# Optimization experiments

Measured on AMD Instinct MI355X. Metric: run time of the kernel, lower is better.

The kernel has to match this reference:

```python
import jax, jax.numpy as jnp
import numpy as np

B, T, C = 8, 1024, 2048  # batch, seq_len (<= T_MAX=1024), n_embd == dim_att


def setup_inputs() -> dict:
    key = jax.random.key(0)
    ks = jax.random.split(key, 10)
    inp = {
        "x": jax.random.normal(ks[0], (B, T, C), dtype=jnp.float32),
        "time_decay": jax.random.normal(ks[1], (C,), dtype=jnp.float32),
        "time_first": jax.random.normal(ks[2], (C,), dtype=jnp.float32),
        "time_mix_k": jax.random.uniform(ks[3], (C,), dtype=jnp.float32),
        "time_mix_v": jax.random.uniform(ks[4], (C,), dtype=jnp.float32),
        "time_mix_r": jax.random.uniform(ks[5], (C,), dtype=jnp.float32),
        "Wk": jax.random.normal(ks[6], (C, C), dtype=jnp.float32) / np.sqrt(C),
        "Wv": jax.random.normal(ks[7], (C, C), dtype=jnp.float32) / np.sqrt(C),
        "Wr": jax.random.normal(ks[8], (C, C), dtype=jnp.float32) / np.sqrt(C),
        "Wo": jax.random.normal(ks[9], (C, C), dtype=jnp.float32) / np.sqrt(C),
    }
    return inp


def _wkv(time_decay, time_first, k, v):
    # Numerically-stabilized RWKV linear-attention recurrence (rwkv_linear_attention_cpu).
    # k, v: [B, T, C]; state tracked in float32.
    w = -jnp.exp(time_decay.astype(jnp.float32))  # [C]
    u = time_first.astype(jnp.float32)            # [C]
    kf = k.astype(jnp.float32)
    vf = v.astype(jnp.float32)

    def step(carry, kv):
        num, den, mx = carry           # each [B, C]
        kt, vt = kv                    # each [B, C]
        max_out = jnp.maximum(mx, kt + u)
        e1 = jnp.exp(mx - max_out)
        e2 = jnp.exp(kt + u - max_out)
        out = (e1 * num + e2 * vt) / (e1 * den + e2)
        max_st = jnp.maximum(mx + w, kt)
        e1s = jnp.exp(mx + w - max_st)
        e2s = jnp.exp(kt - max_st)
        return (e1s * num + e2s * vt, e1s * den + e2s, max_st), out

    Bn, Tn, Cn = k.shape
    init = (jnp.zeros((Bn, Cn), jnp.float32),
            jnp.zeros((Bn, Cn), jnp.float32),
            jnp.full((Bn, Cn), -1e38, jnp.float32))
    kT = jnp.swapaxes(kf, 0, 1)  # [T, B, C]
    vT = jnp.swapaxes(vf, 0, 1)
    _, outs = jax.lax.scan(step, init, (kT, vT))
    return jnp.swapaxes(outs, 0, 1).astype(k.dtype)  # [B, T, C]


def reference(x, time_decay, time_first, time_mix_k, time_mix_v, time_mix_r, Wk, Wv, Wr, Wo):
    # time_shift: shift sequence right by one, zero at t=0
    shifted = jnp.pad(x, ((0, 0), (1, 0), (0, 0)))[:, :-1]
    xk = x * time_mix_k + shifted * (1.0 - time_mix_k)
    xv = x * time_mix_v + shifted * (1.0 - time_mix_v)
    xr = x * time_mix_r + shifted * (1.0 - time_mix_r)
    k = jnp.einsum('btc,dc->btd', xk, Wk)
    v = jnp.einsum('btc,dc->btd', xv, Wv)
    r = jnp.einsum('btc,dc->btd', xr, Wr)
    sr = jax.nn.sigmoid(r)
    rwkv = _wkv(time_decay, time_first, k, v)
    return jnp.einsum('btd,cd->btc', sr * rwkv, Wo)
```

## Files before the change

### kernel.cpp

```cpp
#include <hip/hip_runtime.h>
#include <stdint.h>

#define B_DIM 8
#define T_DIM 1024
#define C_DIM 2048
#define M_DIM (B_DIM * T_DIM)
#define SEG   32
#define SEGL  (T_DIM / SEG)

typedef __bf16 bf16x8 __attribute__((ext_vector_type(8)));
typedef __bf16 bf16x4 __attribute__((ext_vector_type(4)));
typedef float  f32x4  __attribute__((ext_vector_type(4)));

__device__ __forceinline__ void gld_lds16(const void* g, void* l) {
    __builtin_amdgcn_global_load_lds((__attribute__((address_space(1))) void*)g,
                                     (__attribute__((address_space(3))) void*)l,
                                     16, 0, 0);
}

__global__ __launch_bounds__(256) void cast_w_kernel(
    const float* __restrict__ w0, const float* __restrict__ w1,
    const float* __restrict__ w2, const float* __restrict__ w3,
    __bf16* __restrict__ dst) {
    const float* srcs[4] = {w0, w1, w2, w3};
    const float* s = srcs[blockIdx.y];
    __bf16* d = dst + (size_t)blockIdx.y * (size_t)C_DIM * C_DIM;
    const size_t i = ((size_t)blockIdx.x * 256 + threadIdx.x) * 4;
    f32x4 v = *(const f32x4*)(s + i);
    bf16x4 o;
#pragma unroll
    for (int j = 0; j < 4; ++j) o[j] = (__bf16)v[j];
    *(bf16x4*)(d + i) = o;
}

__global__ __launch_bounds__(256) void mix4_kernel(
    const float* __restrict__ x,
    const float* __restrict__ mk, const float* __restrict__ mv,
    const float* __restrict__ mr,
    __bf16* __restrict__ xk, __bf16* __restrict__ xv, __bf16* __restrict__ xr) {
    const size_t idx = ((size_t)blockIdx.x * 256 + threadIdx.x) * 4;
    const int c = (int)(idx & (C_DIM - 1));
    const int t = (int)((idx >> 11) & (T_DIM - 1));

    f32x4 xc = *(const f32x4*)(x + idx);
    f32x4 sh = {0.f, 0.f, 0.f, 0.f};
    if (t != 0) sh = *(const f32x4*)(x + idx - C_DIM);
    f32x4 k4 = *(const f32x4*)(mk + c);
    f32x4 v4 = *(const f32x4*)(mv + c);
    f32x4 r4 = *(const f32x4*)(mr + c);

    bf16x4 ok, ov, orr;
#pragma unroll
    for (int j = 0; j < 4; ++j) {
        float xx = xc[j], ss = sh[j];
        ok[j]  = (__bf16)(xx * k4[j] + ss * (1.f - k4[j]));
        ov[j]  = (__bf16)(xx * v4[j] + ss * (1.f - v4[j]));
        orr[j] = (__bf16)(xx * r4[j] + ss * (1.f - r4[j]));
    }
    *(bf16x4*)(xk + idx) = ok;
    *(bf16x4*)(xv + idx) = ov;
    *(bf16x4*)(xr + idx) = orr;
}

#define LGKM(N)  do { asm volatile("s_waitcnt lgkmcnt(" #N ")" ::: "memory"); \
                      __builtin_amdgcn_sched_barrier(0); } while (0)
#define VM0()    asm volatile("s_waitcnt vmcnt(0)" ::: "memory")

#define MF1(mi, jj, AV, BV) \
    acc[mi][jj] = __builtin_amdgcn_mfma_f32_16x16x32_bf16(AV, BV, acc[mi][jj], 0, 0, 0)

#define MFMA16(MB, AA, BB)                                                        \
    __builtin_amdgcn_s_setprio(1);                                                \
    MF1(MB+0,0,AA[0],BB[0]); MF1(MB+0,1,AA[0],BB[1]);                             \
    MF1(MB+0,2,AA[0],BB[2]); MF1(MB+0,3,AA[0],BB[3]);                             \
    MF1(MB+1,0,AA[1],BB[0]); MF1(MB+1,1,AA[1],BB[1]);                             \
    MF1(MB+1,2,AA[1],BB[2]); MF1(MB+1,3,AA[1],BB[3]);                             \
    MF1(MB+2,0,AA[2],BB[0]); MF1(MB+2,1,AA[2],BB[1]);                             \
    MF1(MB+2,2,AA[2],BB[2]); MF1(MB+2,3,AA[2],BB[3]);                             \
    MF1(MB+3,0,AA[3],BB[0]); MF1(MB+3,1,AA[3],BB[1]);                             \
    MF1(MB+3,2,AA[3],BB[2]); MF1(MB+3,3,AA[3],BB[3]);                             \
    __builtin_amdgcn_s_setprio(0)

#define STAGE8(KOF, BOE)                                                          \
    do {                                                                          \
        gld_lds16(Ag + (KOF),                       lA + (BOE));                  \
        gld_lds16(Bg + (KOF),                       lB + (BOE));                  \
        gld_lds16(Ag + (KOF) + (size_t)64*C_DIM,    lA + (BOE) + 4096);           \
        gld_lds16(Bg + (KOF) + (size_t)64*C_DIM,    lB + (BOE) + 4096);           \
        gld_lds16(Ag + (KOF) + (size_t)128*C_DIM,   lA + (BOE) + 8192);           \
        gld_lds16(Bg + (KOF) + (size_t)128*C_DIM,   lB + (BOE) + 8192);           \
        gld_lds16(Ag + (KOF) + (size_t)192*C_DIM,   lA + (BOE) + 12288);          \
        gld_lds16(Bg + (KOF) + (size_t)192*C_DIM,   lB + (BOE) + 12288);          \
    } while (0)

template <bool OUTF32>
__global__ __launch_bounds__(512, 2) void gemm256_bt(
    const __bf16* __restrict__ A, const __bf16* __restrict__ W,
    void* __restrict__ Cout) {
    __shared__ __align__(16) __bf16 sA[2 * 16384];
    __shared__ __align__(16) __bf16 sB[2 * 16384];

    const int tid  = threadIdx.x;
    const int lane = tid & 63;
    const int wave = tid >> 6;
    const int wr   = wave >> 2;
    const int wc   = wave & 3;

    const int bid = blockIdx.x;
    const int wid = (bid & 7) * 32 + (bid >> 3);
    const int m_blk = wid & 31;
    const int n_blk = wid >> 5;
    const int row0 = m_blk * 256;
    const int col0 = n_blk * 256;

    const int srow = tid >> 3;
    const int sg   = (tid & 7) ^ (srow & 7);
    const __bf16* Ag = A + (size_t)(row0 + srow) * C_DIM + sg * 8;
    const __bf16* Bg = W + (size_t)(col0 + srow) * C_DIM + sg * 8;
    __bf16* lA = sA + wave * 512;
    __bf16* lB = sB + wave * 512;

    const int l15 = lane & 15;
    const int q   = lane >> 4;
    const int sw0 = (q ^ (l15 & 7)) * 8;
    const int aE0 = wr * 8192 + l15 * 64 + sw0;
    const int aE1 = aE0 ^ 32;
    const int bE0 = wc * 4096 + l15 * 64 + sw0;
    const int bE1 = bE0 ^ 32;

    f32x4  acc[8][4] = {};
    bf16x8 a0[4], a1[4], b0f[4], b1f[4];

    STAGE8(0, 0);
    VM0();
    __builtin_amdgcn_s_barrier();
#pragma unroll
    for (int i = 0; i < 4; ++i) a0[i]  = *(const bf16x8*)(sA + aE0 + i * 1024);
#pragma unroll
    for (int j = 0; j < 4; ++j) b0f[j] = *(const bf16x8*)(sB + bE0 + j * 1024);

#pragma unroll 1
    for (int s = 0; s < 31; ++s) {
        const int boe  = (s & 1) << 14;
        const int boe1 = boe ^ 16384;

#pragma unroll
        for (int i = 0; i < 4; ++i)
            a1[i] = *(const bf16x8*)(sA + boe + aE0 + 4096 + i * 1024);
        STAGE8((s + 1) * 64, boe1);
        LGKM(4);
        MFMA16(0, a0, b0f);

#pragma unroll
        for (int i = 0; i < 4; ++i)
            a0[i]  = *(const bf16x8*)(sA + boe + aE1 + i * 1024);
#pragma unroll
        for (int j = 0; j < 4; ++j)
            b1f[j] = *(const bf16x8*)(sB + boe + bE1 + j * 1024);
        LGKM(8);
        MFMA16(4, a1, b0f);

#pragma unroll
        for (int i = 0; i < 4; ++i)
            a1[i] = *(const bf16x8*)(sA + boe + aE1 + 4096 + i * 1024);
        VM0();
        LGKM(4);
        MFMA16(0, a0, b1f);
        __builtin_amdgcn_s_barrier();

#pragma unroll
        for (int i = 0; i < 4; ++i)
            a0[i]  = *(const bf16x8*)(sA + boe1 + aE0 + i * 1024);
#pragma unroll
        for (int j = 0; j < 4; ++j)
            b0f[j] = *(const bf16x8*)(sB + boe1 + bE0 + j * 1024);
        LGKM(8);
        MFMA16(4, a1, b1f);
        __builtin_amdgcn_s_barrier();
    }

    {
        const int boe = 16384;
#pragma unroll
        for (int i = 0; i < 4; ++i)
            a1[i] = *(const bf16x8*)(sA + boe + aE0 + 4096 + i * 1024);
        LGKM(4);
        MFMA16(0, a0, b0f);
#pragma unroll
        for (int i = 0; i < 4; ++i)
            a0[i]  = *(const bf16x8*)(sA + boe + aE1 + i * 1024);
#pragma unroll
        for (int j = 0; j < 4; ++j)
            b1f[j] = *(const bf16x8*)(sB + boe + bE1 + j * 1024);
        LGKM(8);
        MFMA16(4, a1, b0f);
#pragma unroll
        for (int i = 0; i < 4; ++i)
            a1[i] = *(const bf16x8*)(sA + boe + aE1 + 4096 + i * 1024);
        LGKM(4);
        MFMA16(0, a0, b1f);
        LGKM(0);
        MFMA16(4, a1, b1f);
    }

    const int crow = (lane >> 4) * 4;
#pragma unroll
    for (int mf = 0; mf < 8; ++mf)
#pragma unroll
        for (int jf = 0; jf < 4; ++jf)
#pragma unroll
            for (int r = 0; r < 4; ++r) {
                const int row = row0 + wr * 128 + mf * 16 + crow + r;
                const int col = col0 + wc * 64 + jf * 16 + l15;
                if constexpr (OUTF32) {
                    ((float*)Cout)[(size_t)row * C_DIM + col] = acc[mf][jf][r];
                } else {
                    ((__bf16*)Cout)[(size_t)row * C_DIM + col] = (__bf16)acc[mf][jf][r];
                }
            }
}

__global__ __launch_bounds__(256) void wkv_pass1(
    const __bf16* __restrict__ kbuf, const __bf16* __restrict__ vbuf,
    const float* __restrict__ td,
    float* __restrict__ st_num, float* __restrict__ st_den,
    float* __restrict__ st_m) {
    const int c = blockIdx.x * 256 + threadIdx.x;
    const int b = blockIdx.y;
    const int s = blockIdx.z;
    const size_t base = (size_t)b * T_DIM * C_DIM + (size_t)s * SEGL * C_DIM + c;

    const float w = -__expf(td[c]);
    float num = 0.f, den = 0.f, mx = -1e38f;

    for (int t0 = 0; t0 < SEGL; t0 += 8) {
        float kt[8], vt[8];
#pragma unroll
        for (int j = 0; j < 8; ++j) {
            const size_t idx = base + (size_t)(t0 + j) * C_DIM;
            kt[j] = (float)kbuf[idx];
            vt[j] = (float)vbuf[idx];
        }
#pragma unroll
        for (int j = 0; j < 8; ++j) {
            float ms  = fmaxf(mx + w, kt[j]);
            float e1s = __expf(mx + w - ms);
            float e2s = __expf(kt[j] - ms);
            num = e1s * num + e2s * vt[j];
            den = e1s * den + e2s;
            mx  = ms;
        }
    }
    const size_t sidx = (size_t)s * (B_DIM * C_DIM) + (size_t)b * C_DIM + c;
    st_num[sidx] = num;
    st_den[sidx] = den;
    st_m[sidx]   = mx;
}

__global__ __launch_bounds__(256) void wkv_pass2(
    const float* __restrict__ td,
    float* __restrict__ st_num, float* __restrict__ st_den,
    float* __restrict__ st_m) {
    const int bc = blockIdx.x * 256 + threadIdx.x;
    const int c  = bc & (C_DIM - 1);
    const float w = -__expf(td[c]);
    const float wL = w * SEGL;

    float num = 0.f, den = 0.f, mx = -1e38f;
    for (int s = 0; s < SEG; ++s) {
        const size_t sidx = (size_t)s * (B_DIM * C_DIM) + bc;
        float na = st_num[sidx], da = st_den[sidx], ma = st_m[sidx];
        st_num[sidx] = num; st_den[sidx] = den; st_m[sidx] = mx;
        float md = mx + wL;
        float mc = fmaxf(md, ma);
        float e1 = __expf(md - mc);
        float e2 = __expf(ma - mc);
        num = e1 * num + e2 * na;
        den = e1 * den + e2 * da;
        mx  = mc;
    }
}

__global__ __launch_bounds__(256) void wkv_pass3(
    const __bf16* __restrict__ kbuf, const __bf16* __restrict__ vbuf,
    const __bf16* __restrict__ rbuf, const float* __restrict__ td,
    const float* __restrict__ tf,
    const float* __restrict__ st_num, const float* __restrict__ st_den,
    const float* __restrict__ st_m, __bf16* __restrict__ abuf) {
    const int c = blockIdx.x * 256 + threadIdx.x;
    const int b = blockIdx.y;
    const int s = blockIdx.z;
    const size_t base = (size_t)b * T_DIM * C_DIM + (size_t)s * SEGL * C_DIM + c;

    const float w = -__expf(td[c]);
    const float u = tf[c];
    const size_t sidx = (size_t)s * (B_DIM * C_DIM) + (size_t)b * C_DIM + c;
    float num = st_num[sidx], den = st_den[sidx], mx = st_m[sidx];

    for (int t0 = 0; t0 < SEGL; t0 += 8) {
        float kt[8], vt[8], rt[8];
#pragma unroll
        for (int j = 0; j < 8; ++j) {
            const size_t idx = base + (size_t)(t0 + j) * C_DIM;
            kt[j] = (float)kbuf[idx];
            vt[j] = (float)vbuf[idx];
            rt[j] = (float)rbuf[idx];
        }
#pragma unroll
        for (int j = 0; j < 8; ++j) {
            float mo  = fmaxf(mx, kt[j] + u);
            float e1  = __expf(mx - mo);
            float e2  = __expf(kt[j] + u - mo);
            float out = (e1 * num + e2 * vt[j]) / (e1 * den + e2);

            float ms  = fmaxf(mx + w, kt[j]);
            float e1s = __expf(mx + w - ms);
            float e2s = __expf(kt[j] - ms);
            num = e1s * num + e2s * vt[j];
            den = e1s * den + e2s;
            mx  = ms;

            float sr = 1.f / (1.f + __expf(-rt[j]));
            abuf[base + (size_t)(t0 + j) * C_DIM] = (__bf16)(sr * out);
        }
    }
}

extern "C" void kernel_launch(void* const* d_in, const int* in_sizes, int n_in,
                              void* d_out, int out_size, void* d_ws, size_t ws_size,
                              hipStream_t stream) {
    (void)in_sizes; (void)n_in; (void)out_size; (void)ws_size;
    const float* x  = (const float*)d_in[0];
    const float* td = (const float*)d_in[1];
    const float* tf = (const float*)d_in[2];
    const float* mk = (const float*)d_in[3];
    const float* mv = (const float*)d_in[4];
    const float* mr = (const float*)d_in[5];
    const float* Wk = (const float*)d_in[6];
    const float* Wv = (const float*)d_in[7];
    const float* Wr = (const float*)d_in[8];
    const float* Wo = (const float*)d_in[9];
    float* out = (float*)d_out;

    const size_t WN = (size_t)C_DIM * C_DIM;
    const size_t n  = (size_t)M_DIM * C_DIM;

    __bf16* Wb  = (__bf16*)d_ws;
    __bf16* Wkb = Wb;
    __bf16* Wvb = Wb + WN;
    __bf16* Wrb = Wb + 2 * WN;
    __bf16* Wob = Wb + 3 * WN;
    __bf16* xk  = Wb + 4 * WN;
    __bf16* xv  = xk + n;
    __bf16* xr  = xv + n;
    __bf16* kb  = xr + n;
    __bf16* vb  = xk;
    __bf16* rb  = xv;
    __bf16* ab  = xr;

    float* st_num = (float*)d_ws;
    float* st_den = st_num + (size_t)SEG * B_DIM * C_DIM;
    float* st_m   = st_den + (size_t)SEG * B_DIM * C_DIM;

    cast_w_kernel<<<dim3((unsigned)(WN / 4 / 256), 4), 256, 0, stream>>>(
        Wk, Wv, Wr, Wo, Wb);

    mix4_kernel<<<dim3((unsigned)(n / 4 / 256)), 256, 0, stream>>>(
        x, mk, mv, mr, xk, xv, xr);

    dim3 ggrid((M_DIM / 256) * (C_DIM / 256));
    gemm256_bt<false><<<ggrid, 512, 0, stream>>>(xk, Wkb, kb);
    gemm256_bt<false><<<ggrid, 512, 0, stream>>>(xv, Wvb, vb);
    gemm256_bt<false><<<ggrid, 512, 0, stream>>>(xr, Wrb, rb);

    dim3 wgrid(C_DIM / 256, B_DIM, SEG);
    wkv_pass1<<<wgrid, 256, 0, stream>>>(kb, vb, td, st_num, st_den, st_m);
    wkv_pass2<<<dim3(B_DIM * C_DIM / 256), 256, 0, stream>>>(
        td, st_num, st_den, st_m);
    wkv_pass3<<<wgrid, 256, 0, stream>>>(kb, vb, rb, td, tf,
                                         st_num, st_den, st_m, ab);

    gemm256_bt<true><<<ggrid, 512, 0, stream>>>(ab, Wob, out);
}
```

Measured before the change: 514.7 us.

## Replace direct global-to-LDS loads with register-staged prefetch and single LDS buffer

```diff
diff --git a/kernel.cpp b/kernel.cpp
--- a/kernel.cpp
+++ b/kernel.cpp
@@ -11,12 +11,6 @@
 typedef __bf16 bf16x8 __attribute__((ext_vector_type(8)));
 typedef __bf16 bf16x4 __attribute__((ext_vector_type(4)));
 typedef float  f32x4  __attribute__((ext_vector_type(4)));
-
-__device__ __forceinline__ void gld_lds16(const void* g, void* l) {
-    __builtin_amdgcn_global_load_lds((__attribute__((address_space(1))) void*)g,
-                                     (__attribute__((address_space(3))) void*)l,
-                                     16, 0, 0);
-}
 
 __global__ __launch_bounds__(256) void cast_w_kernel(
     const float* __restrict__ w0, const float* __restrict__ w1,
@@ -64,7 +58,10 @@
 
 #define LGKM(N)  do { asm volatile("s_waitcnt lgkmcnt(" #N ")" ::: "memory"); \
                       __builtin_amdgcn_sched_barrier(0); } while (0)
-#define VM0()    asm volatile("s_waitcnt vmcnt(0)" ::: "memory")
+#define LGKM0()  do { asm volatile("s_waitcnt lgkmcnt(0)" ::: "memory"); \
+                      __builtin_amdgcn_sched_barrier(0); } while (0)
+#define VMCNT0() asm volatile("s_waitcnt vmcnt(0)" ::: "memory")
+#define VMCNT8() asm volatile("s_waitcnt vmcnt(8)" ::: "memory")
 
 #define MF1(mi, jj, AV, BV) \
     acc[mi][jj] = __builtin_amdgcn_mfma_f32_16x16x32_bf16(AV, BV, acc[mi][jj], 0, 0, 0)
@@ -81,30 +78,81 @@
     MF1(MB+3,2,AA[3],BB[2]); MF1(MB+3,3,AA[3],BB[3]);                             \
     __builtin_amdgcn_s_setprio(0)
 
-#define STAGE8(KOF, BOE)                                                          \
+#define ISSUE(T, SA, SB)                                                          \
+    do { const __bf16* ap_ = Ag + (size_t)(T) * 64;                               \
+         const __bf16* bp_ = Bg + (size_t)(T) * 64;                               \
+         SA[0] = *(const bf16x8*)(ap_);                                           \
+         SA[1] = *(const bf16x8*)(ap_ + (size_t)64  * C_DIM);                     \
+         SA[2] = *(const bf16x8*)(ap_ + (size_t)128 * C_DIM);                     \
+         SA[3] = *(const bf16x8*)(ap_ + (size_t)192 * C_DIM);                     \
+         SB[0] = *(const bf16x8*)(bp_);                                           \
+         SB[1] = *(const bf16x8*)(bp_ + (size_t)64  * C_DIM);                     \
+         SB[2] = *(const bf16x8*)(bp_ + (size_t)128 * C_DIM);                     \
+         SB[3] = *(const bf16x8*)(bp_ + (size_t)192 * C_DIM); } while (0)
+
+#define DSWRITE(SA, SB)                                                           \
+    do { *(bf16x8*)(sA + wbase)         = SA[0];                                  \
+         *(bf16x8*)(sA + wbase + 4096)  = SA[1];                                  \
+         *(bf16x8*)(sA + wbase + 8192)  = SA[2];                                  \
+         *(bf16x8*)(sA + wbase + 12288) = SA[3];                                  \
+         *(bf16x8*)(sB + wbase)         = SB[0];                                  \
+         *(bf16x8*)(sB + wbase + 4096)  = SB[1];                                  \
+         *(bf16x8*)(sB + wbase + 8192)  = SB[2];                                  \
+         *(bf16x8*)(sB + wbase + 12288) = SB[3]; } while (0)
+
+#define PRELOAD()                                                                 \
+    do { a0[0]  = *(const bf16x8*)(sA + aE0);                                     \
+         a0[1]  = *(const bf16x8*)(sA + aE0 + 1024);                              \
+         a0[2]  = *(const bf16x8*)(sA + aE0 + 2048);                              \
+         a0[3]  = *(const bf16x8*)(sA + aE0 + 3072);                              \
+         b0f[0] = *(const bf16x8*)(sB + bE0);                                     \
+         b0f[1] = *(const bf16x8*)(sB + bE0 + 1024);                              \
+         b0f[2] = *(const bf16x8*)(sB + bE0 + 2048);                              \
+         b0f[3] = *(const bf16x8*)(sB + bE0 + 3072); } while (0)
+
+#define COMPUTE4()                                                                \
     do {                                                                          \
-        gld_lds16(Ag + (KOF),                       lA + (BOE));                  \
-        gld_lds16(Bg + (KOF),                       lB + (BOE));                  \
-        gld_lds16(Ag + (KOF) + (size_t)64*C_DIM,    lA + (BOE) + 4096);           \
-        gld_lds16(Bg + (KOF) + (size_t)64*C_DIM,    lB + (BOE) + 4096);           \
-        gld_lds16(Ag + (KOF) + (size_t)128*C_DIM,   lA + (BOE) + 8192);           \
-        gld_lds16(Bg + (KOF) + (size_t)128*C_DIM,   lB + (BOE) + 8192);           \
-        gld_lds16(Ag + (KOF) + (size_t)192*C_DIM,   lA + (BOE) + 12288);          \
-        gld_lds16(Bg + (KOF) + (size_t)192*C_DIM,   lB + (BOE) + 12288);          \
+        a1[0] = *(const bf16x8*)(sA + aE0 + 4096);                                \
+        a1[1] = *(const bf16x8*)(sA + aE0 + 5120);                                \
+        a1[2] = *(const bf16x8*)(sA + aE0 + 6144);                                \
+        a1[3] = *(const bf16x8*)(sA + aE0 + 7168);                                \
+        LGKM(4);                                                                  \
+        MFMA16(0, a0, b0f);                                                       \
+        a0[0]  = *(const bf16x8*)(sA + aE1);                                      \
+        a0[1]  = *(const bf16x8*)(sA + aE1 + 1024);                               \
+        a0[2]  = *(const bf16x8*)(sA + aE1 + 2048);                               \
+        a0[3]  = *(const bf16x8*)(sA + aE1 + 3072);                               \
+        b1f[0] = *(const bf16x8*)(sB + bE1);                                      \
+        b1f[1] = *(const bf16x8*)(sB + bE1 + 1024);                               \
+        b1f[2] = *(const bf16x8*)(sB + bE1 + 2048);                               \
+        b1f[3] = *(const bf16x8*)(sB + bE1 + 3072);                               \
+        LGKM(8);                                                                  \
+        MFMA16(4, a1, b0f);                                                       \
+        a1[0] = *(const bf16x8*)(sA + aE1 + 4096);                                \
+        a1[1] = *(const bf16x8*)(sA + aE1 + 5120);                                \
+        a1[2] = *(const bf16x8*)(sA + aE1 + 6144);                                \
+        a1[3] = *(const bf16x8*)(sA + aE1 + 7168);                                \
+        LGKM(4);                                                                  \
+        MFMA16(0, a0, b1f);                                                       \
+        LGKM0();                                                                  \
+        MFMA16(4, a1, b1f);                                                       \
     } while (0)
 
 template <bool OUTF32>
 __global__ __launch_bounds__(512, 2) void gemm256_bt(
     const __bf16* __restrict__ A, const __bf16* __restrict__ W,
     void* __restrict__ Cout) {
-    __shared__ __align__(16) __bf16 sA[2 * 16384];
-    __shared__ __align__(16) __bf16 sB[2 * 16384];
+    __shared__ __align__(16) __bf16 sA[16384];
+    __shared__ __align__(16) __bf16 sB[16384];
+    __shared__ __align__(16) __bf16 pad[16384];
 
     const int tid  = threadIdx.x;
     const int lane = tid & 63;
     const int wave = tid >> 6;
     const int wr   = wave >> 2;
     const int wc   = wave & 3;
+
+    if (blockIdx.x == 0xFFFFFFFFu) pad[0] = (__bf16)0.f;
 
     const int bid = blockIdx.x;
     const int wid = (bid & 7) * 32 + (bid >> 3);
@@ -114,11 +162,10 @@
     const int col0 = n_blk * 256;
 
     const int srow = tid >> 3;
-    const int sg   = (tid & 7) ^ (srow & 7);
+    const int sg   = tid & 7;
     const __bf16* Ag = A + (size_t)(row0 + srow) * C_DIM + sg * 8;
     const __bf16* Bg = W + (size_t)(col0 + srow) * C_DIM + sg * 8;
-    __bf16* lA = sA + wave * 512;
-    __bf16* lB = sB + wave * 512;
+    const int wbase = srow * 64 + ((sg ^ (srow & 7)) * 8);
 
     const int l15 = lane & 15;
     const int q   = lane >> 4;
@@ -130,78 +177,45 @@
 
     f32x4  acc[8][4] = {};
     bf16x8 a0[4], a1[4], b0f[4], b1f[4];
-
-    STAGE8(0, 0);
-    VM0();
+    bf16x8 S0A[4], S0B[4], S1A[4], S1B[4];
+
+    ISSUE(0, S0A, S0B);
+    ISSUE(1, S1A, S1B);
+    VMCNT8();
+    DSWRITE(S0A, S0B);
+    LGKM0();
     __builtin_amdgcn_s_barrier();
-#pragma unroll
-    for (int i = 0; i < 4; ++i) a0[i]  = *(const bf16x8*)(sA + aE0 + i * 1024);
-#pragma unroll
-    for (int j = 0; j < 4; ++j) b0f[j] = *(const bf16x8*)(sB + bE0 + j * 1024);
+    PRELOAD();
 
 #pragma unroll 1
-    for (int s = 0; s < 31; ++s) {
-        const int boe  = (s & 1) << 14;
-        const int boe1 = boe ^ 16384;
-
-#pragma unroll
-        for (int i = 0; i < 4; ++i)
-            a1[i] = *(const bf16x8*)(sA + boe + aE0 + 4096 + i * 1024);
-        STAGE8((s + 1) * 64, boe1);
-        LGKM(4);
-        MFMA16(0, a0, b0f);
-
-#pragma unroll
-        for (int i = 0; i < 4; ++i)
-            a0[i]  = *(const bf16x8*)(sA + boe + aE1 + i * 1024);
-#pragma unroll
-        for (int j = 0; j < 4; ++j)
-            b1f[j] = *(const bf16x8*)(sB + boe + bE1 + j * 1024);
-        LGKM(8);
-        MFMA16(4, a1, b0f);
-
-#pragma unroll
-        for (int i = 0; i < 4; ++i)
-            a1[i] = *(const bf16x8*)(sA + boe + aE1 + 4096 + i * 1024);
-        VM0();
-        LGKM(4);
-        MFMA16(0, a0, b1f);
+    for (int p = 0; p < 15; ++p) {
+        const int s = 2 * p;
+        COMPUTE4();
         __builtin_amdgcn_s_barrier();
-
-#pragma unroll
-        for (int i = 0; i < 4; ++i)
-            a0[i]  = *(const bf16x8*)(sA + boe1 + aE0 + i * 1024);
-#pragma unroll
-        for (int j = 0; j < 4; ++j)
-            b0f[j] = *(const bf16x8*)(sB + boe1 + bE0 + j * 1024);
-        LGKM(8);
-        MFMA16(4, a1, b1f);
+        VMCNT0();
+        DSWRITE(S1A, S1B);
+        ISSUE(s + 2, S0A, S0B);
+        LGKM0();
         __builtin_amdgcn_s_barrier();
-    }
-
-    {
-        const int boe = 16384;
-#pragma unroll
-        for (int i = 0; i < 4; ++i)
-            a1[i] = *(const bf16x8*)(sA + boe + aE0 + 4096 + i * 1024);
-        LGKM(4);
-        MFMA16(0, a0, b0f);
-#pragma unroll
-        for (int i = 0; i < 4; ++i)
-            a0[i]  = *(const bf16x8*)(sA + boe + aE1 + i * 1024);
-#pragma unroll
-        for (int j = 0; j < 4; ++j)
-            b1f[j] = *(const bf16x8*)(sB + boe + bE1 + j * 1024);
-        LGKM(8);
-        MFMA16(4, a1, b0f);
-#pragma unroll
-        for (int i = 0; i < 4; ++i)
-            a1[i] = *(const bf16x8*)(sA + boe + aE1 + 4096 + i * 1024);
-        LGKM(4);
-        MFMA16(0, a0, b1f);
-        LGKM(0);
-        MFMA16(4, a1, b1f);
-    }
+        PRELOAD();
+
+        COMPUTE4();
+        __builtin_amdgcn_s_barrier();
+        VMCNT0();
+        DSWRITE(S0A, S0B);
+        ISSUE(s + 3, S1A, S1B);
+        LGKM0();
+        __builtin_amdgcn_s_barrier();
+        PRELOAD();
+    }
+    COMPUTE4();
+    __builtin_amdgcn_s_barrier();
+    VMCNT0();
+    DSWRITE(S1A, S1B);
+    LGKM0();
+    __builtin_amdgcn_s_barrier();
+    PRELOAD();
+    COMPUTE4();
 
     const int crow = (lane >> 4) * 4;
 #pragma unroll
```

New measurement: 581.1 us. 12.9% more time.

## Vectorize WKV scan passes to 4 channels per thread and remap GEMM tiles per XCD

Applied to the files above, without the earlier changes.

```diff
diff --git a/kernel.cpp b/kernel.cpp
--- a/kernel.cpp
+++ b/kernel.cpp
@@ -107,9 +107,10 @@
     const int wc   = wave & 3;
 
     const int bid = blockIdx.x;
-    const int wid = (bid & 7) * 32 + (bid >> 3);
-    const int m_blk = wid & 31;
-    const int n_blk = wid >> 5;
+    const int xcd = bid & 7;
+    const int loc = bid >> 3;
+    const int m_blk = xcd * 4 + (loc & 3);
+    const int n_blk = loc >> 2;
     const int row0 = m_blk * 256;
     const int col0 = n_blk * 256;
 
@@ -225,36 +226,48 @@
     const float* __restrict__ td,
     float* __restrict__ st_num, float* __restrict__ st_den,
     float* __restrict__ st_m) {
-    const int c = blockIdx.x * 256 + threadIdx.x;
+    const int c0 = (blockIdx.x * 256 + threadIdx.x) * 4;
     const int b = blockIdx.y;
     const int s = blockIdx.z;
-    const size_t base = (size_t)b * T_DIM * C_DIM + (size_t)s * SEGL * C_DIM + c;
-
-    const float w = -__expf(td[c]);
-    float num = 0.f, den = 0.f, mx = -1e38f;
+    const size_t base = (size_t)b * T_DIM * C_DIM + (size_t)s * SEGL * C_DIM + c0;
+
+    f32x4 td4 = *(const f32x4*)(td + c0);
+    float w[4], num[4], den[4], mx[4];
+#pragma unroll
+    for (int e = 0; e < 4; ++e) {
+        w[e] = -__expf(td4[e]);
+        num[e] = 0.f; den[e] = 0.f; mx[e] = -1e38f;
+    }
 
     for (int t0 = 0; t0 < SEGL; t0 += 8) {
-        float kt[8], vt[8];
+        bf16x4 kt[8], vt[8];
 #pragma unroll
         for (int j = 0; j < 8; ++j) {
             const size_t idx = base + (size_t)(t0 + j) * C_DIM;
-            kt[j] = (float)kbuf[idx];
-            vt[j] = (float)vbuf[idx];
+            kt[j] = *(const bf16x4*)(kbuf + idx);
+            vt[j] = *(const bf16x4*)(vbuf + idx);
         }
 #pragma unroll
         for (int j = 0; j < 8; ++j) {
-            float ms  = fmaxf(mx + w, kt[j]);
-            float e1s = __expf(mx + w - ms);
-            float e2s = __expf(kt[j] - ms);
-            num = e1s * num + e2s * vt[j];
-            den = e1s * den + e2s;
-            mx  = ms;
+#pragma unroll
+            for (int e = 0; e < 4; ++e) {
+                float kk = (float)kt[j][e], vv = (float)vt[j][e];
+                float ms  = fmaxf(mx[e] + w[e], kk);
+                float e1s = __expf(mx[e] + w[e] - ms);
+                float e2s = __expf(kk - ms);
+                num[e] = e1s * num[e] + e2s * vv;
+                den[e] = e1s * den[e] + e2s;
+                mx[e]  = ms;
+            }
         }
     }
-    const size_t sidx = (size_t)s * (B_DIM * C_DIM) + (size_t)b * C_DIM + c;
-    st_num[sidx] = num;
-    st_den[sidx] = den;
-    st_m[sidx]   = mx;
+    const size_t sidx = (size_t)s * (B_DIM * C_DIM) + (size_t)b * C_DIM + c0;
+    f32x4 n4, d4, m4;
+#pragma unroll
+    for (int e = 0; e < 4; ++e) { n4[e] = num[e]; d4[e] = den[e]; m4[e] = mx[e]; }
+    *(f32x4*)(st_num + sidx) = n4;
+    *(f32x4*)(st_den + sidx) = d4;
+    *(f32x4*)(st_m   + sidx) = m4;
 }
 
 __global__ __launch_bounds__(256) void wkv_pass2(
@@ -287,41 +300,57 @@
     const float* __restrict__ tf,
     const float* __restrict__ st_num, const float* __restrict__ st_den,
     const float* __restrict__ st_m, __bf16* __restrict__ abuf) {
-    const int c = blockIdx.x * 256 + threadIdx.x;
+    const int c0 = (blockIdx.x * 256 + threadIdx.x) * 4;
     const int b = blockIdx.y;
     const int s = blockIdx.z;
-    const size_t base = (size_t)b * T_DIM * C_DIM + (size_t)s * SEGL * C_DIM + c;
-
-    const float w = -__expf(td[c]);
-    const float u = tf[c];
-    const size_t sidx = (size_t)s * (B_DIM * C_DIM) + (size_t)b * C_DIM + c;
-    float num = st_num[sidx], den = st_den[sidx], mx = st_m[sidx];
+    const size_t base = (size_t)b * T_DIM * C_DIM + (size_t)s * SEGL * C_DIM + c0;
+
+    f32x4 td4 = *(const f32x4*)(td + c0);
+    f32x4 tf4 = *(const f32x4*)(tf + c0);
+    const size_t sidx = (size_t)s * (B_DIM * C_DIM) + (size_t)b * C_DIM + c0;
+    f32x4 n4 = *(const f32x4*)(st_num + sidx);
+    f32x4 d4 = *(const f32x4*)(st_den + sidx);
+    f32x4 m4 = *(const f32x4*)(st_m + sidx);
+
+    float w[4], u[4], num[4], den[4], mx[4];
+#pragma unroll
+    for (int e = 0; e < 4; ++e) {
+        w[e] = -__expf(td4[e]);
+        u[e] = tf4[e];
+        num[e] = n4[e]; den[e] = d4[e]; mx[e] = m4[e];
+    }
 
     for (int t0 = 0; t0 < SEGL; t0 += 8) {
-        float kt[8], vt[8], rt[8];
+        bf16x4 kt[8], vt[8], rt[8];
 #pragma unroll
         for (int j = 0; j < 8; ++j) {
             const size_t idx = base + (size_t)(t0 + j) * C_DIM;
-            kt[j] = (float)kbuf[idx];
-            vt[j] = (float)vbuf[idx];
-            rt[j] = (float)rbuf[idx];
+            kt[j] = *(const bf16x4*)(kbuf + idx);
+            vt[j] = *(const bf16x4*)(vbuf + idx);
+            rt[j] = *(const bf16x4*)(rbuf + idx);
         }
 #pragma unroll
         for (int j = 0; j < 8; ++j) {
-            float mo  = fmaxf(mx, kt[j] + u);
-            float e1  = __expf(mx - mo);
-            float e2  = __expf(kt[j] + u - mo);
-            float out = (e1 * num + e2 * vt[j]) / (e1 * den + e2);
-
-            float ms  = fmaxf(mx + w, kt[j]);
-            float e1s = __expf(mx + w - ms);
-            float e2s = __expf(kt[j] - ms);
-            num = e1s * num + e2s * vt[j];
-            den = e1s * den + e2s;
-            mx  = ms;
-
-            float sr = 1.f / (1.f + __expf(-rt[j]));
-            abuf[base + (size_t)(t0 + j) * C_DIM] = (__bf16)(sr * out);
+            bf16x4 o4;
+#pragma unroll
+            for (int e = 0; e < 4; ++e) {
+                float kk = (float)kt[j][e], vv = (float)vt[j][e], rr = (float)rt[j][e];
+                float mo  = fmaxf(mx[e], kk + u[e]);
+                float e1  = __expf(mx[e] - mo);
+                float e2  = __expf(kk + u[e] - mo);
+                float out = (e1 * num[e] + e2 * vv) / (e1 * den[e] + e2);
+
+                float ms  = fmaxf(mx[e] + w[e], kk);
+                float e1s = __expf(mx[e] + w[e] - ms);
+                float e2s = __expf(kk - ms);
+                num[e] = e1s * num[e] + e2s * vv;
+                den[e] = e1s * den[e] + e2s;
+                mx[e]  = ms;
+
+                float sr = 1.f / (1.f + __expf(-rr));
+                o4[e] = (__bf16)(sr * out);
+            }
+            *(bf16x4*)(abuf + base + (size_t)(t0 + j) * C_DIM) = o4;
         }
     }
 }
@@ -373,7 +402,7 @@
     gemm256_bt<false><<<ggrid, 512, 0, stream>>>(xv, Wvb, vb);
     gemm256_bt<false><<<ggrid, 512, 0, stream>>>(xr, Wrb, rb);
 
-    dim3 wgrid(C_DIM / 256, B_DIM, SEG);
+    dim3 wgrid(C_DIM / 1024, B_DIM, SEG);
     wkv_pass1<<<wgrid, 256, 0, stream>>>(kb, vb, td, st_num, st_den, st_m);
     wkv_pass2<<<dim3(B_DIM * C_DIM / 256), 256, 0, stream>>>(
         td, st_num, st_den, st_m);
```

Measured after the change: 488.2 us. 1.05x faster.
